# Kernel tuning notes

Measured on AMD Instinct MI355X. Metric: run time of the kernel, lower is better.

The kernel has to match this reference:

```python
import jax, jax.numpy as jnp
import numpy as np

B, N_Z, N_E, D = 16, 2048, 2048, 512

def setup_inputs() -> dict:
    key = jax.random.key(0)
    kz, ke, km = jax.random.split(key, 3)
    z = jax.random.normal(kz, (B, N_Z, D), dtype=jnp.float32)
    e = jax.random.normal(ke, (B, N_E, D), dtype=jnp.float32)
    M = jax.random.normal(km, (D, D), dtype=jnp.float32)  # init: normal(0, 1)
    return {"z": z, "e": e, "M": M}

def reference(z, e, M):
    # a = z @ M @ e^T : [B, Nz, Ne]
    zM = jnp.einsum('bnd,de->bne', z, M)
    a = jnp.einsum('bnd,bmd->bnm', zM, e)
    a = jax.nn.sigmoid(a)
    # softmax over dim=1 (the Nz axis), as in the torch code
    A = jax.nn.softmax(a, axis=1)
    # out = A @ e : [B, Nz, D]
    return jnp.einsum('bnm,bmd->bnd', A, e)
```

## Files before the change

### kernel.cpp

```cpp
#include <hip/hip_runtime.h>
#include <hip/hip_bf16.h>
#include <stdint.h>

#define BB 16
#define NZ 2048
#define NE 2048
#define DD 512

typedef unsigned short u16;
typedef __attribute__((ext_vector_type(8))) _Float16 f16x8;
typedef __attribute__((ext_vector_type(4))) float f32x4;

__device__ __forceinline__ u16 f2h(float f) {
  _Float16 h = (_Float16)f;
  return __builtin_bit_cast(u16, h);
}

__device__ __forceinline__ void gload_lds16(const void* g, void* l) {
  auto gp = (const __attribute__((address_space(1))) uint32_t*)g;
  auto lp = (__attribute__((address_space(3))) uint32_t*)l;
  __builtin_amdgcn_global_load_lds(gp, lp, 16, 0, 0);
}

__global__ void k_cvt(const float* __restrict__ in, u16* __restrict__ out, int n4) {
  int i = blockIdx.x * blockDim.x + threadIdx.x;
  int stride = gridDim.x * blockDim.x;
  for (; i < n4; i += stride) {
    float4 v = ((const float4*)in)[i];
    ushort4 o;
    o.x = f2h(v.x); o.y = f2h(v.y); o.z = f2h(v.z); o.w = f2h(v.w);
    ((ushort4*)out)[i] = o;
  }
}

__global__ void k_mt(const float* __restrict__ M, u16* __restrict__ Mt) {
  __shared__ float t[32][33];
  int bx = blockIdx.x * 32;
  int by = blockIdx.y * 32;
  for (int r = 0; r < 32; r += 8)
    t[threadIdx.y + r][threadIdx.x] = M[(size_t)(by + threadIdx.y + r) * DD + bx + threadIdx.x];
  __syncthreads();
  for (int r = 0; r < 32; r += 8)
    Mt[(size_t)(bx + threadIdx.y + r) * DD + by + threadIdx.x] = f2h(t[threadIdx.x][threadIdx.y + r]);
}

__global__ void k_et(const float* __restrict__ e, const float* __restrict__ cs,
                     u16* __restrict__ eT) {
  __shared__ float t[32][33];
  int b = blockIdx.z;
  int m0 = blockIdx.y * 32, d0 = blockIdx.x * 32;
  const float* eb = e + (size_t)b * NE * DD;
  const float* csb = cs + (size_t)b * NE;
  for (int r = 0; r < 32; r += 8) {
    int m = m0 + threadIdx.y + r;
    t[threadIdx.y + r][threadIdx.x] =
        eb[(size_t)m * DD + d0 + threadIdx.x] * (2048.0f / csb[m]);
  }
  __syncthreads();
  u16* eTb = eT + (size_t)b * DD * NE;
  for (int r = 0; r < 32; r += 8) {
    int d = d0 + threadIdx.y + r;
    eTb[(size_t)d * NE + m0 + threadIdx.x] = f2h(t[threadIdx.x][threadIdx.y + r]);
  }
}

template<int EPI>
__global__ __launch_bounds__(256, 2) void k_gemm(
    const u16* __restrict__ A, const u16* __restrict__ Bt, void* __restrict__ Cp,
    int Ndim, int K, long long sAb, long long sBb, long long sCb,
    float* __restrict__ colsum, int csld)
{
  const int tid = threadIdx.x;
  const int lane = tid & 63;
  const int wid = tid >> 6;
  const int wr = wid >> 1, wc = wid & 1;
  const int bz = blockIdx.z;
  const int row0 = blockIdx.y * 128;
  const int col0 = blockIdx.x * 128;

  const u16* Ab = A + (long long)bz * sAb;
  const u16* Bb = Bt + (long long)bz * sBb;

  __shared__ u16 As[2][128 * 32];
  __shared__ u16 Bs[2][128 * 32];

  f32x4 acc[4][4] = {};

  const int rA = lane & 15;
  const int kq = (lane >> 4) * 8;

  const int nk = K >> 5;
  int cur = 0;

  auto stage = [&](int buf, int kt) {
    const int k0 = kt * 32;
#pragma unroll
    for (int c = 0; c < 2; ++c) {
      int q = c * 256 + tid;
      int r = q >> 2, col = (q & 3) * 8;
      gload_lds16(Ab + (long long)(row0 + r) * K + k0 + col,
                  (char*)(&As[buf][0]) + (c * 256 + wid * 64) * 16);
      gload_lds16(Bb + (long long)(col0 + r) * K + k0 + col,
                  (char*)(&Bs[buf][0]) + (c * 256 + wid * 64) * 16);
    }
  };

  stage(0, 0);
  for (int kt = 0; kt < nk; ++kt) {
    __syncthreads();
    if (kt + 1 < nk) stage(cur ^ 1, kt + 1);
    const u16* as = &As[cur][0];
    const u16* bs = &Bs[cur][0];
    f16x8 af[4], bfr[4];
#pragma unroll
    for (int m = 0; m < 4; ++m)
      af[m] = *(const f16x8*)(as + (wr * 64 + m * 16 + rA) * 32 + kq);
#pragma unroll
    for (int n = 0; n < 4; ++n)
      bfr[n] = *(const f16x8*)(bs + (wc * 64 + n * 16 + rA) * 32 + kq);
#pragma unroll
    for (int m = 0; m < 4; ++m)
#pragma unroll
      for (int n = 0; n < 4; ++n)
        acc[m][n] = __builtin_amdgcn_mfma_f32_16x16x32_f16(af[m], bfr[n], acc[m][n], 0, 0, 0);
    cur ^= 1;
  }

  if constexpr (EPI == 0) {
    u16* C = (u16*)Cp + (long long)bz * sCb;
#pragma unroll
    for (int m = 0; m < 4; ++m)
#pragma unroll
      for (int n = 0; n < 4; ++n)
#pragma unroll
        for (int j = 0; j < 4; ++j) {
          int row = row0 + wr * 64 + m * 16 + (lane >> 4) * 4 + j;
          int col = col0 + wc * 64 + n * 16 + (lane & 15);
          C[(long long)row * Ndim + col] = f2h(acc[m][n][j]);
        }
  } else if constexpr (EPI == 1) {
    u16* C = (u16*)Cp + (long long)bz * sCb;
    float csum[4] = {0.f, 0.f, 0.f, 0.f};
#pragma unroll
    for (int m = 0; m < 4; ++m)
#pragma unroll
      for (int n = 0; n < 4; ++n)
#pragma unroll
        for (int j = 0; j < 4; ++j) {
          float x = acc[m][n][j];
          float s = 1.f / (1.f + __expf(-x));
          float v = __expf(s);
          int row = row0 + wr * 64 + m * 16 + (lane >> 4) * 4 + j;
          int col = col0 + wc * 64 + n * 16 + (lane & 15);
          C[(long long)row * Ndim + col] = f2h(v);
          csum[n] += v;
        }
#pragma unroll
    for (int n = 0; n < 4; ++n) {
      float v = csum[n];
      v += __shfl_xor(v, 16, 64);
      v += __shfl_xor(v, 32, 64);
      if ((lane >> 4) == 0)
        atomicAdd(&colsum[(long long)bz * csld + col0 + wc * 64 + n * 16 + (lane & 15)], v);
    }
  } else {
    float* C = (float*)Cp + (long long)bz * sCb;
#pragma unroll
    for (int m = 0; m < 4; ++m)
#pragma unroll
      for (int n = 0; n < 4; ++n)
#pragma unroll
        for (int j = 0; j < 4; ++j) {
          int row = row0 + wr * 64 + m * 16 + (lane >> 4) * 4 + j;
          int col = col0 + wc * 64 + n * 16 + (lane & 15);
          C[(long long)row * Ndim + col] = acc[m][n][j] * (1.0f / 2048.0f);
        }
  }
}

extern "C" void kernel_launch(void* const* d_in, const int* in_sizes, int n_in,
                              void* d_out, int out_size, void* d_ws, size_t ws_size,
                              hipStream_t stream) {
  const float* z = (const float*)d_in[0];
  const float* e = (const float*)d_in[1];
  const float* M = (const float*)d_in[2];
  float* out = (float*)d_out;
  char* ws = (char*)d_ws;

  u16* S    = (u16*)(ws + 0LL);
  u16* zM   = (u16*)(ws + 134217728LL);
  u16* zH   = (u16*)(ws + 167772160LL);
  u16* eH   = (u16*)(ws + 201326592LL);
  u16* Mt   = (u16*)(ws + 234881024LL);
  float* cs = (float*)(ws + 235405312LL);

  hipMemsetAsync(cs, 0, (size_t)BB * NE * sizeof(float), stream);

  k_cvt<<<4096, 256, 0, stream>>>(z, zH, BB * NZ * DD / 4);
  k_cvt<<<4096, 256, 0, stream>>>(e, eH, BB * NE * DD / 4);
  k_mt<<<dim3(16, 16), dim3(32, 8), 0, stream>>>(M, Mt);

  k_gemm<0><<<dim3(DD / 128, (BB * NZ) / 128, 1), 256, 0, stream>>>(
      zH, Mt, zM, DD, DD, 0LL, 0LL, 0LL, nullptr, 0);

  k_gemm<1><<<dim3(NE / 128, NZ / 128, BB), 256, 0, stream>>>(
      zM, eH, S, NE, DD,
      (long long)NZ * DD, (long long)NE * DD, (long long)NZ * NE, cs, NE);

  u16* eT = zH;
  k_et<<<dim3(DD / 32, NE / 32, BB), dim3(32, 8), 0, stream>>>(e, cs, eT);

  k_gemm<2><<<dim3(DD / 128, NZ / 128, BB), 256, 0, stream>>>(
      S, eT, out, DD, NE,
      (long long)NZ * NE, (long long)DD * NE, (long long)NZ * DD, nullptr, 0);
}
```

Baseline: 332.1 us.

## Rewrite GEMM as 256x256 tile, 8-wave kernel with pipelined LDS staging

The shared GEMM kernel moves from 128x128 tiles with 4 waves to 256x256 tiles with 8 waves and a K-step of 64. Operands are staged into 128KB of dynamic LDS in an MFMA-fragment-ordered layout, using explicit vmcnt/lgkmcnt waits, raw barriers and setprio around the MFMA blocks so the next tile's global loads overlap compute. Workgroups are remapped across XCDs for better L2 locality, and K is now a compile-time template parameter. The larger tiles raise data reuse but cut the number of workgroups and may limit occupancy, and the hand-written waitcnt logic is fragile.

```diff
diff --git a/kernel.cpp b/kernel.cpp
--- a/kernel.cpp
+++ b/kernel.cpp
@@ -21,6 +21,12 @@
   auto lp = (__attribute__((address_space(3))) uint32_t*)l;
   __builtin_amdgcn_global_load_lds(gp, lp, 16, 0, 0);
 }
+
+#define FENCE() asm volatile("" ::: "memory")
+#define BARRIER() do { FENCE(); __builtin_amdgcn_s_barrier(); FENCE(); } while (0)
+#define WAIT_LGKM0() do { asm volatile("s_waitcnt lgkmcnt(0)" ::: "memory"); \
+                          __builtin_amdgcn_sched_barrier(0); } while (0)
+#define WAIT_VM(n) asm volatile("s_waitcnt vmcnt(" #n ")" ::: "memory")
 
 __global__ void k_cvt(const float* __restrict__ in, u16* __restrict__ out, int n4) {
   int i = blockIdx.x * blockDim.x + threadIdx.x;
@@ -64,85 +70,149 @@
   }
 }
 
-template<int EPI>
-__global__ __launch_bounds__(256, 2) void k_gemm(
+template<int EPI, int KDIM>
+__global__ __launch_bounds__(512, 2) void k_gemm(
     const u16* __restrict__ A, const u16* __restrict__ Bt, void* __restrict__ Cp,
-    int Ndim, int K, long long sAb, long long sBb, long long sCb,
+    int Ndim, long long sAb, long long sBb, long long sCb,
     float* __restrict__ colsum, int csld)
 {
+  extern __shared__ char lds[];
+  constexpr int NT = KDIM / 64;
+
+  const int gx = gridDim.x, gy = gridDim.y;
+  const int nwg = gx * gy * gridDim.z;
+  const int hid = blockIdx.x + gx * (blockIdx.y + gy * blockIdx.z);
+  const int logical = (hid & 7) * (nwg >> 3) + (hid >> 3);
+  const int bx = logical % gx;
+  const int rem0 = logical / gx;
+  const int by = rem0 % gy;
+  const int bz = rem0 / gy;
+
   const int tid = threadIdx.x;
   const int lane = tid & 63;
   const int wid = tid >> 6;
-  const int wr = wid >> 1, wc = wid & 1;
-  const int bz = blockIdx.z;
-  const int row0 = blockIdx.y * 128;
-  const int col0 = blockIdx.x * 128;
+  const int wr = wid >> 2;
+  const int wc = wid & 3;
+
+  const int row0 = by * 256;
+  const int col0 = bx * 256;
 
   const u16* Ab = A + (long long)bz * sAb;
   const u16* Bb = Bt + (long long)bz * sBb;
 
-  __shared__ u16 As[2][128 * 32];
-  __shared__ u16 Bs[2][128 * 32];
-
-  f32x4 acc[4][4] = {};
-
-  const int rA = lane & 15;
-  const int kq = (lane >> 4) * 8;
-
-  const int nk = K >> 5;
-  int cur = 0;
-
-  auto stage = [&](int buf, int kt) {
-    const int k0 = kt * 32;
-#pragma unroll
-    for (int c = 0; c < 2; ++c) {
-      int q = c * 256 + tid;
-      int r = q >> 2, col = (q & 3) * 8;
-      gload_lds16(Ab + (long long)(row0 + r) * K + k0 + col,
-                  (char*)(&As[buf][0]) + (c * 256 + wid * 64) * 16);
-      gload_lds16(Bb + (long long)(col0 + r) * K + k0 + col,
-                  (char*)(&Bs[buf][0]) + (c * 256 + wid * 64) * 16);
+  const u16* srcA[4]; const u16* srcB[4];
+#pragma unroll
+  for (int c = 0; c < 4; ++c) {
+    int idx = c * 512 + tid;
+    int ks = idx >> 10, rm = idx & 1023;
+    int mf = rm >> 6, q = (rm >> 4) & 3, p = rm & 15;
+    int r = mf * 16 + p, c8 = ks * 4 + q;
+    srcA[c] = Ab + (long long)(row0 + r) * KDIM + c8 * 8;
+    srcB[c] = Bb + (long long)(col0 + r) * KDIM + c8 * 8;
+  }
+
+  auto stage = [&](int buf, int k0) {
+#pragma unroll
+    for (int c = 0; c < 4; ++c) {
+      gload_lds16(srcA[c] + k0, lds + buf * 32768 + (c * 512 + wid * 64) * 16);
+      gload_lds16(srcB[c] + k0, lds + 65536 + buf * 32768 + (c * 512 + wid * 64) * 16);
     }
   };
 
+  auto ldA = [&](int buf, int ks, int m) -> f16x8 {
+    return *(const f16x8*)(lds + buf * 32768 +
+                           ((ks * 16 + wr * 8 + m) * 64 + lane) * 16);
+  };
+  auto ldB = [&](int buf, int ks, int n) -> f16x8 {
+    return *(const f16x8*)(lds + 65536 + buf * 32768 +
+                           ((ks * 16 + wc * 4 + n) * 64 + lane) * 16);
+  };
+
+  f32x4 acc[8][4] = {};
+  f16x8 af[4], bf[4];
+
   stage(0, 0);
-  for (int kt = 0; kt < nk; ++kt) {
-    __syncthreads();
-    if (kt + 1 < nk) stage(cur ^ 1, kt + 1);
-    const u16* as = &As[cur][0];
-    const u16* bs = &Bs[cur][0];
-    f16x8 af[4], bfr[4];
-#pragma unroll
-    for (int m = 0; m < 4; ++m)
-      af[m] = *(const f16x8*)(as + (wr * 64 + m * 16 + rA) * 32 + kq);
-#pragma unroll
-    for (int n = 0; n < 4; ++n)
-      bfr[n] = *(const f16x8*)(bs + (wc * 64 + n * 16 + rA) * 32 + kq);
-#pragma unroll
-    for (int m = 0; m < 4; ++m)
-#pragma unroll
-      for (int n = 0; n < 4; ++n)
-        acc[m][n] = __builtin_amdgcn_mfma_f32_16x16x32_f16(af[m], bfr[n], acc[m][n], 0, 0, 0);
-    cur ^= 1;
-  }
-
+  WAIT_VM(4);
+  BARRIER();
+
+  for (int t = 0; t < NT; ++t) {
+    const int buf = t & 1;
+#pragma unroll
+    for (int m = 0; m < 4; ++m) af[m] = ldA(buf, 0, m);
+#pragma unroll
+    for (int n = 0; n < 4; ++n) bf[n] = ldB(buf, 0, n);
+    if (t + 1 < NT) stage(buf ^ 1, (t + 1) * 64);
+    BARRIER();
+    WAIT_LGKM0();
+    __builtin_amdgcn_s_setprio(1);
+#pragma unroll
+    for (int m = 0; m < 4; ++m)
+#pragma unroll
+      for (int n = 0; n < 4; ++n)
+        acc[m][n] = __builtin_amdgcn_mfma_f32_16x16x32_f16(af[m], bf[n], acc[m][n], 0, 0, 0);
+    __builtin_amdgcn_s_setprio(0);
+    BARRIER();
+#pragma unroll
+    for (int m = 0; m < 4; ++m) af[m] = ldA(buf, 0, 4 + m);
+    BARRIER();
+    WAIT_LGKM0();
+    __builtin_amdgcn_s_setprio(1);
+#pragma unroll
+    for (int m = 0; m < 4; ++m)
+#pragma unroll
+      for (int n = 0; n < 4; ++n)
+        acc[4 + m][n] = __builtin_amdgcn_mfma_f32_16x16x32_f16(af[m], bf[n], acc[4 + m][n], 0, 0, 0);
+    __builtin_amdgcn_s_setprio(0);
+    if (t + 1 < NT) { WAIT_VM(8); } else { WAIT_VM(0); }
+    BARRIER();
+#pragma unroll
+    for (int m = 0; m < 4; ++m) af[m] = ldA(buf, 1, m);
+#pragma unroll
+    for (int n = 0; n < 4; ++n) bf[n] = ldB(buf, 1, n);
+    BARRIER();
+    WAIT_LGKM0();
+    __builtin_amdgcn_s_setprio(1);
+#pragma unroll
+    for (int m = 0; m < 4; ++m)
+#pragma unroll
+      for (int n = 0; n < 4; ++n)
+        acc[m][n] = __builtin_amdgcn_mfma_f32_16x16x32_f16(af[m], bf[n], acc[m][n], 0, 0, 0);
+    __builtin_amdgcn_s_setprio(0);
+    BARRIER();
+#pragma unroll
+    for (int m = 0; m < 4; ++m) af[m] = ldA(buf, 1, 4 + m);
+    BARRIER();
+    WAIT_LGKM0();
+    __builtin_amdgcn_s_setprio(1);
+#pragma unroll
+    for (int m = 0; m < 4; ++m)
+#pragma unroll
+      for (int n = 0; n < 4; ++n)
+        acc[4 + m][n] = __builtin_amdgcn_mfma_f32_16x16x32_f16(af[m], bf[n], acc[4 + m][n], 0, 0, 0);
+    __builtin_amdgcn_s_setprio(0);
+    if (t + 1 < NT) { WAIT_VM(4); }
+    BARRIER();
+  }
+
+  const int rr = (lane >> 4) * 4;
+  const int cc = lane & 15;
   if constexpr (EPI == 0) {
     u16* C = (u16*)Cp + (long long)bz * sCb;
 #pragma unroll
-    for (int m = 0; m < 4; ++m)
+    for (int m = 0; m < 8; ++m)
 #pragma unroll
       for (int n = 0; n < 4; ++n)
 #pragma unroll
         for (int j = 0; j < 4; ++j) {
-          int row = row0 + wr * 64 + m * 16 + (lane >> 4) * 4 + j;
-          int col = col0 + wc * 64 + n * 16 + (lane & 15);
+          int row = row0 + wr * 128 + m * 16 + rr + j;
+          int col = col0 + wc * 64 + n * 16 + cc;
           C[(long long)row * Ndim + col] = f2h(acc[m][n][j]);
         }
   } else if constexpr (EPI == 1) {
     u16* C = (u16*)Cp + (long long)bz * sCb;
     float csum[4] = {0.f, 0.f, 0.f, 0.f};
 #pragma unroll
-    for (int m = 0; m < 4; ++m)
+    for (int m = 0; m < 8; ++m)
 #pragma unroll
       for (int n = 0; n < 4; ++n)
 #pragma unroll
@@ -150,8 +220,8 @@
           float x = acc[m][n][j];
           float s = 1.f / (1.f + __expf(-x));
           float v = __expf(s);
-          int row = row0 + wr * 64 + m * 16 + (lane >> 4) * 4 + j;
-          int col = col0 + wc * 64 + n * 16 + (lane & 15);
+          int row = row0 + wr * 128 + m * 16 + rr + j;
+          int col = col0 + wc * 64 + n * 16 + cc;
           C[(long long)row * Ndim + col] = f2h(v);
           csum[n] += v;
         }
@@ -161,18 +231,18 @@
       v += __shfl_xor(v, 16, 64);
       v += __shfl_xor(v, 32, 64);
       if ((lane >> 4) == 0)
-        atomicAdd(&colsum[(long long)bz * csld + col0 + wc * 64 + n * 16 + (lane & 15)], v);
+        atomicAdd(&colsum[(long long)bz * csld + col0 + wc * 64 + n * 16 + cc], v);
     }
   } else {
     float* C = (float*)Cp + (long long)bz * sCb;
 #pragma unroll
-    for (int m = 0; m < 4; ++m)
+    for (int m = 0; m < 8; ++m)
 #pragma unroll
       for (int n = 0; n < 4; ++n)
 #pragma unroll
         for (int j = 0; j < 4; ++j) {
-          int row = row0 + wr * 64 + m * 16 + (lane >> 4) * 4 + j;
-          int col = col0 + wc * 64 + n * 16 + (lane & 15);
+          int row = row0 + wr * 128 + m * 16 + rr + j;
+          int col = col0 + wc * 64 + n * 16 + cc;
           C[(long long)row * Ndim + col] = acc[m][n][j] * (1.0f / 2048.0f);
         }
   }
@@ -194,23 +264,30 @@
   u16* Mt   = (u16*)(ws + 234881024LL);
   float* cs = (float*)(ws + 235405312LL);
 
+  (void)hipFuncSetAttribute(reinterpret_cast<const void*>(&k_gemm<0, 512>),
+                            hipFuncAttributeMaxDynamicSharedMemorySize, 131072);
+  (void)hipFuncSetAttribute(reinterpret_cast<const void*>(&k_gemm<1, 512>),
+                            hipFuncAttributeMaxDynamicSharedMemorySize, 131072);
+  (void)hipFuncSetAttribute(reinterpret_cast<const void*>(&k_gemm<2, 2048>),
+                            hipFuncAttributeMaxDynamicSharedMemorySize, 131072);
+
   hipMemsetAsync(cs, 0, (size_t)BB * NE * sizeof(float), stream);
 
   k_cvt<<<4096, 256, 0, stream>>>(z, zH, BB * NZ * DD / 4);
   k_cvt<<<4096, 256, 0, stream>>>(e, eH, BB * NE * DD / 4);
   k_mt<<<dim3(16, 16), dim3(32, 8), 0, stream>>>(M, Mt);
 
-  k_gemm<0><<<dim3(DD / 128, (BB * NZ) / 128, 1), 256, 0, stream>>>(
-      zH, Mt, zM, DD, DD, 0LL, 0LL, 0LL, nullptr, 0);
-
-  k_gemm<1><<<dim3(NE / 128, NZ / 128, BB), 256, 0, stream>>>(
-      zM, eH, S, NE, DD,
+  k_gemm<0, 512><<<dim3(DD / 256, (BB * NZ) / 256, 1), 512, 131072, stream>>>(
+      zH, Mt, zM, DD, 0LL, 0LL, 0LL, nullptr, 0);
+
+  k_gemm<1, 512><<<dim3(NE / 256, NZ / 256, BB), 512, 131072, stream>>>(
+      zM, eH, S, NE,
       (long long)NZ * DD, (long long)NE * DD, (long long)NZ * NE, cs, NE);
 
   u16* eT = zH;
   k_et<<<dim3(DD / 32, NE / 32, BB), dim3(32, 8), 0, stream>>>(e, cs, eT);
 
-  k_gemm<2><<<dim3(DD / 128, NZ / 128, BB), 256, 0, stream>>>(
-      S, eT, out, DD, NE,
+  k_gemm<2, 2048><<<dim3(DD / 256, NZ / 256, BB), 512, 131072, stream>>>(
+      S, eT, out, DD,
       (long long)NZ * NE, (long long)DD * NE, (long long)NZ * DD, nullptr, 0);
 }
```

Result: no change. 326.3 us (-1.7%).
